# Optimization experiments

Measured on AMD Instinct MI355X. Metric: run time of the kernel, lower is better.

Reference implementation:

```python
import jax, jax.numpy as jnp
import numpy as np

B, S, D = 8, 1024, 1024
H = 2048            # expert hidden dim
E = 8               # num experts
TOP_K = 2
D_NOISE = 256
TEMP = 1.0


def setup_inputs() -> dict:
    key = jax.random.key(0)
    ks = jax.random.split(key, 8)
    return {
        "x": jax.random.normal(ks[0], (B, S, D), dtype=jnp.float32),
        "noise_clock_emb": jax.random.normal(ks[1], (B, D_NOISE), dtype=jnp.float32),
        # router weight [D_noise, E] (xavier-ish scale)
        "route_weight": jax.random.normal(ks[2], (D_NOISE, E), dtype=jnp.float32) * (1.0 / np.sqrt(D_NOISE)),
        # stacked expert params; torch Linear y = x @ W.T + b, stored here pre-transposed
        "fc_in_w": jax.random.normal(ks[3], (E, D, 2 * H), dtype=jnp.float32) * 0.02,
        "fc_in_b": jax.random.normal(ks[4], (E, 2 * H), dtype=jnp.float32) * 0.02,
        "fc_out_w": jax.random.normal(ks[5], (E, H, D), dtype=jnp.float32) * 0.02,
        "fc_out_b": jax.random.normal(ks[6], (E, D), dtype=jnp.float32) * 0.02,
    }


def reference(x, noise_clock_emb, route_weight, fc_in_w, fc_in_b, fc_out_w, fc_out_b):
    # ---- router: P = softmax(phi(sigma) @ W_R / T) ----
    logits = (noise_clock_emb @ route_weight) / TEMP            # [B, E]
    probs = jax.nn.softmax(logits, axis=-1)
    topk_weights, topk_indices = jax.lax.top_k(probs, TOP_K)    # [B, K]
    topk_weights = topk_weights / jnp.clip(
        topk_weights.sum(axis=-1, keepdims=True), 1e-8)
    # dense per-(batch, expert) mixing coefficient, identical to the
    # masked accumulation in the torch loop
    coeff = jnp.einsum("bke,bk->be",
                       jax.nn.one_hot(topk_indices, E, dtype=x.dtype),
                       topk_weights)                             # [B, E]

    # ---- all experts densely over the full batch (matches original math) ----
    h = jnp.einsum("bsd,edh->ebsh", x, fc_in_w) + fc_in_b[:, None, None, :]
    value, gate = jnp.split(h, 2, axis=-1)                       # [E,B,S,H] each
    hidden = value * jax.nn.silu(gate)
    mixed = jnp.einsum("ebsh,ehd,be->bsd", hidden, fc_out_w, coeff)
    mixed = mixed + jnp.einsum("be,ed->bd", coeff, fc_out_b)[:, None, :]
    return mixed, logits, probs, topk_indices, topk_weights
```

## Files before the change

kernel.cpp:

```cpp
#include <hip/hip_runtime.h>
#include <stdint.h>

#define B_ 8
#define S_ 1024
#define D_ 1024
#define H_ 2048
#define E_ 8
#define DN_ 256

typedef unsigned char u8;
typedef unsigned int u32;
typedef float f32x4 __attribute__((ext_vector_type(4)));
typedef long long ll;

__device__ __forceinline__ u8 f2f8(float f) {
  return (u8)(__builtin_amdgcn_cvt_pk_fp8_f32(f, f, 0, false) & 0xff);
}
__device__ __forceinline__ u32 pk4f8(float a, float b, float c, float d) {
  int w = __builtin_amdgcn_cvt_pk_fp8_f32(a, b, 0, false);
  w = __builtin_amdgcn_cvt_pk_fp8_f32(c, d, w, true);
  return (u32)w;
}

__device__ __forceinline__ void gll16(const void* g, void* l) {
  __builtin_amdgcn_global_load_lds(
      (__attribute__((address_space(1))) void*)g,
      (__attribute__((address_space(3))) void*)l, 16, 0, 0);
}

template <int R, int C>
__device__ __forceinline__ void transpose_body(const float* __restrict__ ip,
                                               u8* __restrict__ op,
                                               int bx, int by, int t,
                                               u32 (&tl)[64][65]) {
  const int r0 = by * 256, c0 = bx * 64;
  const int rg16 = t >> 4;
  const int cg = t & 15;
#pragma unroll
  for (int p = 0; p < 4; ++p) {
    const int rq = p * 16 + rg16;
    const float* q = ip + (size_t)(r0 + rq * 4) * C + c0 + cg * 4;
    float4 v0 = *(const float4*)(q);
    float4 v1 = *(const float4*)(q + C);
    float4 v2 = *(const float4*)(q + 2 * C);
    float4 v3 = *(const float4*)(q + 3 * C);
    tl[cg * 4 + 0][rq] = pk4f8(v0.x, v1.x, v2.x, v3.x);
    tl[cg * 4 + 1][rq] = pk4f8(v0.y, v1.y, v2.y, v3.y);
    tl[cg * 4 + 2][rq] = pk4f8(v0.z, v1.z, v2.z, v3.z);
    tl[cg * 4 + 3][rq] = pk4f8(v0.w, v1.w, v2.w, v3.w);
  }
  __syncthreads();
  const int ch = t & 15;
#pragma unroll
  for (int p = 0; p < 4; ++p) {
    const int c = p * 16 + (t >> 4);
    uint4 w;
    w.x = tl[c][ch * 4 + 0];
    w.y = tl[c][ch * 4 + 1];
    w.z = tl[c][ch * 4 + 2];
    w.w = tl[c][ch * 4 + 3];
    *(uint4*)(op + (size_t)(c0 + c) * R + r0 + ch * 16) = w;
  }
}

#define NCAST (B_ * S_ * D_ / 1024)
#define NT1 ((2 * H_ / 64) * (D_ / 256) * E_)
#define NT2 ((D_ / 64) * (H_ / 256) * E_)

__global__ void __launch_bounds__(256) prep_kernel(
    const float* __restrict__ x, const float* __restrict__ noise,
    const float* __restrict__ rw, const float* __restrict__ fiw,
    const float* __restrict__ fow,
    float* __restrict__ out_logits, float* __restrict__ out_probs,
    float* __restrict__ out_idx, float* __restrict__ out_w,
    int* __restrict__ ws_idx, float* __restrict__ ws_w,
    u32* __restrict__ xq, u8* __restrict__ wtin,
    u8* __restrict__ wtout) {
  __shared__ __align__(16) u32 tile[64][65];
  const int t = threadIdx.x;
  int bid = blockIdx.x;

  if (bid == 0) {
    float* sl = (float*)&tile[0][0];
    float* sp = sl + 64;
    {
      const int pair = t >> 2, sub = t & 3;
      const int b = pair >> 3, e = pair & 7;
      float acc = 0.f;
      const int d0 = sub * 64;
      for (int d = d0; d < d0 + 64; ++d)
        acc += noise[b * DN_ + d] * rw[d * E_ + e];
      acc += __shfl_xor(acc, 1);
      acc += __shfl_xor(acc, 2);
      if (sub == 0) sl[pair] = acc;
    }
    __syncthreads();
    if (t < 64) {
      const int b = t >> 3;
      float L = sl[t];
      out_logits[t] = L;
      float m = -1e30f;
      for (int j = 0; j < 8; ++j) m = fmaxf(m, sl[b * 8 + j]);
      float s = 0.f;
      for (int j = 0; j < 8; ++j) s += __expf(sl[b * 8 + j] - m);
      float p = __expf(L - m) / s;
      out_probs[t] = p;
      sp[t] = p;
    }
    __syncthreads();
    if (t < 64 && (t & 7) == 0) {
      const int b = t >> 3;
      int a1 = 0; float v1 = sp[b * 8];
      for (int j = 1; j < 8; ++j) { float v = sp[b * 8 + j]; if (v > v1) { v1 = v; a1 = j; } }
      int a2 = -1; float v2 = -1e30f;
      for (int j = 0; j < 8; ++j) {
        if (j == a1) continue;
        float v = sp[b * 8 + j]; if (v > v2) { v2 = v; a2 = j; }
      }
      float sum = fmaxf(v1 + v2, 1e-8f);
      float w1 = v1 / sum, w2 = v2 / sum;
      out_idx[b * 2] = (float)a1; out_idx[b * 2 + 1] = (float)a2;
      out_w[b * 2] = w1; out_w[b * 2 + 1] = w2;
      ws_idx[b * 2] = a1; ws_idx[b * 2 + 1] = a2;
      ws_w[b * 2] = w1; ws_w[b * 2 + 1] = w2;
    }
    return;
  }
  bid -= 1;
  if (bid < NCAST) {
    const size_t i = (size_t)bid * 256 + t;
    float4 v = *((const float4*)x + i);
    xq[i] = pk4f8(v.x, v.y, v.z, v.w);
    return;
  }
  bid -= NCAST;
  if (bid < NT1) {
    const int bx = bid & 63, by = (bid >> 6) & 3, e = bid >> 8;
    transpose_body<D_, 2 * H_>(fiw + (size_t)e * D_ * 2 * H_,
                               wtin + (size_t)e * D_ * 2 * H_, bx, by, t, tile);
    return;
  }
  bid -= NT1;
  {
    const int bx = bid & 15, by = (bid >> 4) & 7, e = bid >> 7;
    transpose_body<H_, D_>(fow + (size_t)e * H_ * D_,
                           wtout + (size_t)e * H_ * D_, bx, by, t, tile);
  }
}

__global__ void __launch_bounds__(256, 4) gemm1_kernel(
    const u8* __restrict__ xq,
    const u8* __restrict__ wtin,
    const float* __restrict__ bin,
    const int* __restrict__ ws_idx, const float* __restrict__ ws_w,
    u8* __restrict__ hid)
{
  const int nt = blockIdx.x;
  const int mt = blockIdx.y;
  const int z  = blockIdx.z;
  const int b  = z >> 1;
  const int e  = ws_idx[z] & 7;
  const float csc = ws_w[z];

  __shared__ u8 As[128 * 128];
  __shared__ u8 Bs[128 * 128];

  const int t = threadIdx.x;
  const int wave = t >> 6, lane = t & 63;
  const int wm = wave >> 1, wn = wave & 1;
  const int lm = lane & 15, lq = lane >> 4;
  const int lrow8 = lane >> 3;
  const int kq = ((lane & 7) ^ lrow8) * 16;
  const int fsw = lm & 7;
  const int p0 = lq >> 1, fb = (lq & 1) * 8;

  const u8* Ab  = xq + (size_t)b * (S_ * D_) + (size_t)mt * 128 * D_;
  const u8* Bvb = wtin + (size_t)e * (2 * H_ * D_) + (size_t)nt * 64 * D_;
  const u8* Bgb = Bvb + (size_t)H_ * D_;

  const f32x4 vz = {0.f, 0.f, 0.f, 0.f};
  f32x4 accv[4][2], accg[4][2];
#pragma unroll
  for (int i = 0; i < 4; ++i)
#pragma unroll
    for (int j = 0; j < 2; ++j) { accv[i][j] = vz; accg[i][j] = vz; }

  for (int kt = 0; kt < D_ / 128; ++kt) {
    const int k0 = kt * 128 + kq;
    gll16(Ab + (size_t)(wave * 8 + lrow8) * D_ + k0, (char*)As + wave * 1024);
    gll16(Ab + (size_t)((wave + 4) * 8 + lrow8) * D_ + k0, (char*)As + (wave + 4) * 1024);
    gll16(Ab + (size_t)((wave + 8) * 8 + lrow8) * D_ + k0, (char*)As + (wave + 8) * 1024);
    gll16(Ab + (size_t)((wave + 12) * 8 + lrow8) * D_ + k0, (char*)As + (wave + 12) * 1024);
    gll16(Bvb + (size_t)(wave * 8 + lrow8) * D_ + k0, (char*)Bs + wave * 1024);
    gll16(Bvb + (size_t)((wave + 4) * 8 + lrow8) * D_ + k0, (char*)Bs + (wave + 4) * 1024);
    gll16(Bgb + (size_t)(wave * 8 + lrow8) * D_ + k0, (char*)Bs + (8 + wave) * 1024);
    gll16(Bgb + (size_t)((wave + 4) * 8 + lrow8) * D_ + k0, (char*)Bs + (12 + wave) * 1024);
    __syncthreads();
#pragma unroll
    for (int hg = 0; hg < 2; ++hg) {
      ll af[4][2], bvf[2][2], bgf[2][2];
#pragma unroll
      for (int h2 = 0; h2 < 2; ++h2) {
        const int pw = ((((hg * 2 + h2) * 2 + p0) ^ fsw)) * 16 + fb;
#pragma unroll
        for (int i = 0; i < 4; ++i)
          af[i][h2] = *(const ll*)(As + (wm * 64 + i * 16 + lm) * 128 + pw);
#pragma unroll
        for (int j = 0; j < 2; ++j) {
          bvf[j][h2] = *(const ll*)(Bs + (wn * 32 + j * 16 + lm) * 128 + pw);
          bgf[j][h2] = *(const ll*)(Bs + (64 + wn * 32 + j * 16 + lm) * 128 + pw);
        }
      }
#pragma unroll
      for (int h2 = 0; h2 < 2; ++h2)
#pragma unroll
        for (int i = 0; i < 4; ++i)
#pragma unroll
          for (int j = 0; j < 2; ++j) {
            accv[i][j] = __builtin_amdgcn_mfma_f32_16x16x32_fp8_fp8(af[i][h2], bvf[j][h2], accv[i][j], 0, 0, 0);
            accg[i][j] = __builtin_amdgcn_mfma_f32_16x16x32_fp8_fp8(af[i][h2], bgf[j][h2], accg[i][j], 0, 0, 0);
          }
    }
    __syncthreads();
  }

  u8* hb = hid + (size_t)z * (S_ * H_);
  const int row0 = mt * 128 + wm * 64;
  const int col0 = nt * 64 + wn * 32;
#pragma unroll
  for (int j = 0; j < 2; ++j) {
    const int col = col0 + j * 16 + lm;
    const float bvx = bin[e * 2 * H_ + col];
    const float bgx = bin[e * 2 * H_ + H_ + col];
#pragma unroll
    for (int i = 0; i < 4; ++i) {
#pragma unroll
      for (int r = 0; r < 4; ++r) {
        const int srow = row0 + i * 16 + lq * 4 + r;
        float v = accv[i][j][r] + bvx;
        float g = accg[i][j][r] + bgx;
        float hv = v * g / (1.f + __expf(-g)) * csc;
        hb[(size_t)srow * H_ + col] = f2f8(hv);
      }
    }
  }
}

__global__ void __launch_bounds__(256, 4) gemm2_kernel(
    const u8* __restrict__ hid,
    const u8* __restrict__ wtout,
    const float* __restrict__ bout,
    const int* __restrict__ ws_idx, const float* __restrict__ ws_w,
    float* __restrict__ out)
{
  const int nt = blockIdx.x;
  const int mt = blockIdx.y;
  const int b  = blockIdx.z;

  __shared__ u8 As[128 * 128];
  __shared__ u8 Bs[64 * 128];

  const int t = threadIdx.x;
  const int wave = t >> 6, lane = t & 63;
  const int wm = wave >> 1, wn = wave & 1;
  const int lm = lane & 15, lq = lane >> 4;
  const int lrow8 = lane >> 3;
  const int kq = ((lane & 7) ^ lrow8) * 16;
  const int fsw = lm & 7;
  const int p0 = lq >> 1, fb = (lq & 1) * 8;

  const int e0 = ws_idx[b * 2] & 7, e1 = ws_idx[b * 2 + 1] & 7;
  const u8* Ab0 = hid + ((size_t)(b * 2 + 0) * S_ + mt * 128) * H_;
  const u8* Ab1 = hid + ((size_t)(b * 2 + 1) * S_ + mt * 128) * H_;
  const u8* Bb0 = wtout + ((size_t)e0 * D_ + nt * 64) * H_;
  const u8* Bb1 = wtout + ((size_t)e1 * D_ + nt * 64) * H_;

  const f32x4 vz = {0.f, 0.f, 0.f, 0.f};
  f32x4 acc[4][2];
#pragma unroll
  for (int i = 0; i < 4; ++i)
#pragma unroll
    for (int j = 0; j < 2; ++j) acc[i][j] = vz;

  for (int it = 0; it < 32; ++it) {
    const u8* Ab = (it & 16) ? Ab1 : Ab0;
    const u8* Bb = (it & 16) ? Bb1 : Bb0;
    const int k0 = (it & 15) * 128 + kq;
    gll16(Ab + (size_t)(wave * 8 + lrow8) * H_ + k0, (char*)As + wave * 1024);
    gll16(Ab + (size_t)((wave + 4) * 8 + lrow8) * H_ + k0, (char*)As + (wave + 4) * 1024);
    gll16(Ab + (size_t)((wave + 8) * 8 + lrow8) * H_ + k0, (char*)As + (wave + 8) * 1024);
    gll16(Ab + (size_t)((wave + 12) * 8 + lrow8) * H_ + k0, (char*)As + (wave + 12) * 1024);
    gll16(Bb + (size_t)(wave * 8 + lrow8) * H_ + k0, (char*)Bs + wave * 1024);
    gll16(Bb + (size_t)((wave + 4) * 8 + lrow8) * H_ + k0, (char*)Bs + (wave + 4) * 1024);
    __syncthreads();
#pragma unroll
    for (int hg = 0; hg < 2; ++hg) {
      ll af[4][2], bf[2][2];
#pragma unroll
      for (int h2 = 0; h2 < 2; ++h2) {
        const int pw = ((((hg * 2 + h2) * 2 + p0) ^ fsw)) * 16 + fb;
#pragma unroll
        for (int i = 0; i < 4; ++i)
          af[i][h2] = *(const ll*)(As + (wm * 64 + i * 16 + lm) * 128 + pw);
#pragma unroll
        for (int j = 0; j < 2; ++j)
          bf[j][h2] = *(const ll*)(Bs + (wn * 32 + j * 16 + lm) * 128 + pw);
      }
#pragma unroll
      for (int h2 = 0; h2 < 2; ++h2)
#pragma unroll
        for (int i = 0; i < 4; ++i)
#pragma unroll
          for (int j = 0; j < 2; ++j)
            acc[i][j] = __builtin_amdgcn_mfma_f32_16x16x32_fp8_fp8(af[i][h2], bf[j][h2], acc[i][j], 0, 0, 0);
    }
    __syncthreads();
  }

  const float c0 = ws_w[b * 2], c1 = ws_w[b * 2 + 1];
  float* ob = out + (size_t)b * (S_ * D_);
  const int row0 = mt * 128 + wm * 64;
  const int col0 = nt * 64 + wn * 32;
#pragma unroll
  for (int j = 0; j < 2; ++j) {
    const int col = col0 + j * 16 + lm;
    const float bias = c0 * bout[e0 * D_ + col] + c1 * bout[e1 * D_ + col];
#pragma unroll
    for (int i = 0; i < 4; ++i)
#pragma unroll
      for (int r = 0; r < 4; ++r)
        ob[(size_t)(row0 + i * 16 + lq * 4 + r) * D_ + col] = acc[i][j][r] + bias;
  }
}

extern "C" void kernel_launch(void* const* d_in, const int* in_sizes, int n_in,
                              void* d_out, int out_size, void* d_ws, size_t ws_size,
                              hipStream_t stream) {
  const float* x     = (const float*)d_in[0];
  const float* noise = (const float*)d_in[1];
  const float* rw    = (const float*)d_in[2];
  const float* fiw   = (const float*)d_in[3];
  const float* fib   = (const float*)d_in[4];
  const float* fow   = (const float*)d_in[5];
  const float* fob   = (const float*)d_in[6];
  float* out = (float*)d_out;

  char* ws = (char*)d_ws;
  int*   ws_idx = (int*)ws;
  float* ws_w   = (float*)(ws + 64);
  u8* xq    = (u8*)(ws + 256);
  u8* wtin  = xq + (size_t)B_ * S_ * D_;
  u8* wtout = wtin + (size_t)E_ * 2 * H_ * D_;
  u8* hid   = wtout + (size_t)E_ * D_ * H_;

  float* out_mixed  = out;
  float* out_logits = out + (size_t)B_ * S_ * D_;
  float* out_probs  = out_logits + B_ * E_;
  float* out_idx    = out_probs + B_ * E_;
  float* out_w      = out_idx + B_ * 2;

  prep_kernel<<<1 + NCAST + NT1 + NT2, 256, 0, stream>>>(
      x, noise, rw, fiw, fow, out_logits, out_probs, out_idx, out_w,
      ws_idx, ws_w, (u32*)xq, wtin, wtout);
  gemm1_kernel<<<dim3(32, 8, 16), 256, 0, stream>>>(xq, wtin, fib, ws_idx, ws_w, hid);
  gemm2_kernel<<<dim3(16, 8, 8), 256, 0, stream>>>(hid, wtout, fob, ws_idx, ws_w, out_mixed);
}
```

Measured before the change: 425.1 us.

## Share A tile across both selected experts in gemm1 and widen gemm2 N-tile

gemm1 now processes both top-k experts of a batch in one 512-thread block, so the activation tile loaded into shared memory feeds the value and gate projections of both experts. This halves the grid and the activation reloads. gemm2 also moves to 512 threads with a 128-wide output tile, halving its grid and the reloads of the hidden A tile. Each block now uses more LDS (48KB for gemm1) and there are fewer blocks, which could lower occupancy and latency hiding.

```diff
diff --git a/kernel.cpp b/kernel.cpp
--- a/kernel.cpp
+++ b/kernel.cpp
@@ -148,7 +148,7 @@
   }
 }
 
-__global__ void __launch_bounds__(256, 4) gemm1_kernel(
+__global__ void __launch_bounds__(512, 4) gemm1_kernel(
     const u8* __restrict__ xq,
     const u8* __restrict__ wtin,
     const float* __restrict__ bin,
@@ -157,17 +157,16 @@
 {
   const int nt = blockIdx.x;
   const int mt = blockIdx.y;
-  const int z  = blockIdx.z;
-  const int b  = z >> 1;
-  const int e  = ws_idx[z] & 7;
-  const float csc = ws_w[z];
+  const int b  = blockIdx.z;
+  const int e0 = ws_idx[b * 2] & 7, e1 = ws_idx[b * 2 + 1] & 7;
+  const float c0 = ws_w[b * 2], c1 = ws_w[b * 2 + 1];
 
   __shared__ u8 As[128 * 128];
-  __shared__ u8 Bs[128 * 128];
+  __shared__ u8 Bs[256 * 128];
 
   const int t = threadIdx.x;
   const int wave = t >> 6, lane = t & 63;
-  const int wm = wave >> 1, wn = wave & 1;
+  const int wm = wave >> 2, wn = wave & 3;
   const int lm = lane & 15, lq = lane >> 4;
   const int lrow8 = lane >> 3;
   const int kq = ((lane & 7) ^ lrow8) * 16;
@@ -175,78 +174,75 @@
   const int p0 = lq >> 1, fb = (lq & 1) * 8;
 
   const u8* Ab  = xq + (size_t)b * (S_ * D_) + (size_t)mt * 128 * D_;
-  const u8* Bvb = wtin + (size_t)e * (2 * H_ * D_) + (size_t)nt * 64 * D_;
-  const u8* Bgb = Bvb + (size_t)H_ * D_;
+  const u8* Bv0 = wtin + (size_t)e0 * (2 * H_ * D_) + (size_t)nt * 64 * D_;
+  const u8* Bg0 = Bv0 + (size_t)H_ * D_;
+  const u8* Bv1 = wtin + (size_t)e1 * (2 * H_ * D_) + (size_t)nt * 64 * D_;
+  const u8* Bg1 = Bv1 + (size_t)H_ * D_;
 
   const f32x4 vz = {0.f, 0.f, 0.f, 0.f};
-  f32x4 accv[4][2], accg[4][2];
+  f32x4 acc[4][4];
 #pragma unroll
   for (int i = 0; i < 4; ++i)
 #pragma unroll
-    for (int j = 0; j < 2; ++j) { accv[i][j] = vz; accg[i][j] = vz; }
+    for (int j = 0; j < 4; ++j) acc[i][j] = vz;
 
   for (int kt = 0; kt < D_ / 128; ++kt) {
     const int k0 = kt * 128 + kq;
-    gll16(Ab + (size_t)(wave * 8 + lrow8) * D_ + k0, (char*)As + wave * 1024);
-    gll16(Ab + (size_t)((wave + 4) * 8 + lrow8) * D_ + k0, (char*)As + (wave + 4) * 1024);
-    gll16(Ab + (size_t)((wave + 8) * 8 + lrow8) * D_ + k0, (char*)As + (wave + 8) * 1024);
-    gll16(Ab + (size_t)((wave + 12) * 8 + lrow8) * D_ + k0, (char*)As + (wave + 12) * 1024);
-    gll16(Bvb + (size_t)(wave * 8 + lrow8) * D_ + k0, (char*)Bs + wave * 1024);
-    gll16(Bvb + (size_t)((wave + 4) * 8 + lrow8) * D_ + k0, (char*)Bs + (wave + 4) * 1024);
-    gll16(Bgb + (size_t)(wave * 8 + lrow8) * D_ + k0, (char*)Bs + (8 + wave) * 1024);
-    gll16(Bgb + (size_t)((wave + 4) * 8 + lrow8) * D_ + k0, (char*)Bs + (12 + wave) * 1024);
-    __syncthreads();
-#pragma unroll
-    for (int hg = 0; hg < 2; ++hg) {
-      ll af[4][2], bvf[2][2], bgf[2][2];
-#pragma unroll
-      for (int h2 = 0; h2 < 2; ++h2) {
-        const int pw = ((((hg * 2 + h2) * 2 + p0) ^ fsw)) * 16 + fb;
-#pragma unroll
-        for (int i = 0; i < 4; ++i)
-          af[i][h2] = *(const ll*)(As + (wm * 64 + i * 16 + lm) * 128 + pw);
-#pragma unroll
-        for (int j = 0; j < 2; ++j) {
-          bvf[j][h2] = *(const ll*)(Bs + (wn * 32 + j * 16 + lm) * 128 + pw);
-          bgf[j][h2] = *(const ll*)(Bs + (64 + wn * 32 + j * 16 + lm) * 128 + pw);
-        }
+    const size_t rr = (size_t)(wave * 8 + lrow8);
+    gll16(Ab + rr * D_ + k0, (char*)As + wave * 1024);
+    gll16(Ab + (rr + 64) * D_ + k0, (char*)As + (wave + 8) * 1024);
+    gll16(Bv0 + rr * D_ + k0, (char*)Bs + wave * 1024);
+    gll16(Bg0 + rr * D_ + k0, (char*)Bs + (8 + wave) * 1024);
+    gll16(Bv1 + rr * D_ + k0, (char*)Bs + (16 + wave) * 1024);
+    gll16(Bg1 + rr * D_ + k0, (char*)Bs + (24 + wave) * 1024);
+    __syncthreads();
+#pragma unroll
+    for (int ks = 0; ks < 4; ++ks) {
+      const int pw = ((ks * 2 + p0) ^ fsw) * 16 + fb;
+      ll af[4];
+#pragma unroll
+      for (int i = 0; i < 4; ++i)
+        af[i] = *(const ll*)(As + (wm * 64 + i * 16 + lm) * 128 + pw);
+      const int brow = wn * 16 + lm;
+      ll b0v = *(const ll*)(Bs + (brow) * 128 + pw);
+      ll b0g = *(const ll*)(Bs + (64 + brow) * 128 + pw);
+      ll b1v = *(const ll*)(Bs + (128 + brow) * 128 + pw);
+      ll b1g = *(const ll*)(Bs + (192 + brow) * 128 + pw);
+#pragma unroll
+      for (int i = 0; i < 4; ++i) {
+        acc[i][0] = __builtin_amdgcn_mfma_f32_16x16x32_fp8_fp8(af[i], b0v, acc[i][0], 0, 0, 0);
+        acc[i][1] = __builtin_amdgcn_mfma_f32_16x16x32_fp8_fp8(af[i], b0g, acc[i][1], 0, 0, 0);
+        acc[i][2] = __builtin_amdgcn_mfma_f32_16x16x32_fp8_fp8(af[i], b1v, acc[i][2], 0, 0, 0);
+        acc[i][3] = __builtin_amdgcn_mfma_f32_16x16x32_fp8_fp8(af[i], b1g, acc[i][3], 0, 0, 0);
       }
-#pragma unroll
-      for (int h2 = 0; h2 < 2; ++h2)
-#pragma unroll
-        for (int i = 0; i < 4; ++i)
-#pragma unroll
-          for (int j = 0; j < 2; ++j) {
-            accv[i][j] = __builtin_amdgcn_mfma_f32_16x16x32_fp8_fp8(af[i][h2], bvf[j][h2], accv[i][j], 0, 0, 0);
-            accg[i][j] = __builtin_amdgcn_mfma_f32_16x16x32_fp8_fp8(af[i][h2], bgf[j][h2], accg[i][j], 0, 0, 0);
-          }
-    }
-    __syncthreads();
-  }
-
-  u8* hb = hid + (size_t)z * (S_ * H_);
+    }
+    __syncthreads();
+  }
+
+  u8* hb0 = hid + (size_t)(b * 2 + 0) * (S_ * H_);
+  u8* hb1 = hid + (size_t)(b * 2 + 1) * (S_ * H_);
   const int row0 = mt * 128 + wm * 64;
-  const int col0 = nt * 64 + wn * 32;
-#pragma unroll
-  for (int j = 0; j < 2; ++j) {
-    const int col = col0 + j * 16 + lm;
-    const float bvx = bin[e * 2 * H_ + col];
-    const float bgx = bin[e * 2 * H_ + H_ + col];
-#pragma unroll
-    for (int i = 0; i < 4; ++i) {
-#pragma unroll
-      for (int r = 0; r < 4; ++r) {
-        const int srow = row0 + i * 16 + lq * 4 + r;
-        float v = accv[i][j][r] + bvx;
-        float g = accg[i][j][r] + bgx;
-        float hv = v * g / (1.f + __expf(-g)) * csc;
-        hb[(size_t)srow * H_ + col] = f2f8(hv);
-      }
-    }
-  }
-}
-
-__global__ void __launch_bounds__(256, 4) gemm2_kernel(
+  const int col = nt * 64 + wn * 16 + lm;
+  const float bv0 = bin[e0 * 2 * H_ + col];
+  const float bg0 = bin[e0 * 2 * H_ + H_ + col];
+  const float bv1 = bin[e1 * 2 * H_ + col];
+  const float bg1 = bin[e1 * 2 * H_ + H_ + col];
+#pragma unroll
+  for (int i = 0; i < 4; ++i) {
+#pragma unroll
+    for (int r = 0; r < 4; ++r) {
+      const int srow = row0 + i * 16 + lq * 4 + r;
+      float v0 = acc[i][0][r] + bv0;
+      float g0 = acc[i][1][r] + bg0;
+      hb0[(size_t)srow * H_ + col] = f2f8(v0 * g0 / (1.f + __expf(-g0)) * c0);
+      float v1 = acc[i][2][r] + bv1;
+      float g1 = acc[i][3][r] + bg1;
+      hb1[(size_t)srow * H_ + col] = f2f8(v1 * g1 / (1.f + __expf(-g1)) * c1);
+    }
+  }
+}
+
+__global__ void __launch_bounds__(512, 4) gemm2_kernel(
     const u8* __restrict__ hid,
     const u8* __restrict__ wtout,
     const float* __restrict__ bout,
@@ -258,11 +254,11 @@
   const int b  = blockIdx.z;
 
   __shared__ u8 As[128 * 128];
-  __shared__ u8 Bs[64 * 128];
+  __shared__ u8 Bs[128 * 128];
 
   const int t = threadIdx.x;
   const int wave = t >> 6, lane = t & 63;
-  const int wm = wave >> 1, wn = wave & 1;
+  const int wm = wave >> 2, wn = wave & 3;
   const int lm = lane & 15, lq = lane >> 4;
   const int lrow8 = lane >> 3;
   const int kq = ((lane & 7) ^ lrow8) * 16;
@@ -272,8 +268,8 @@
   const int e0 = ws_idx[b * 2] & 7, e1 = ws_idx[b * 2 + 1] & 7;
   const u8* Ab0 = hid + ((size_t)(b * 2 + 0) * S_ + mt * 128) * H_;
   const u8* Ab1 = hid + ((size_t)(b * 2 + 1) * S_ + mt * 128) * H_;
-  const u8* Bb0 = wtout + ((size_t)e0 * D_ + nt * 64) * H_;
-  const u8* Bb1 = wtout + ((size_t)e1 * D_ + nt * 64) * H_;
+  const u8* Bb0 = wtout + ((size_t)e0 * D_ + nt * 128) * H_;
+  const u8* Bb1 = wtout + ((size_t)e1 * D_ + nt * 128) * H_;
 
   const f32x4 vz = {0.f, 0.f, 0.f, 0.f};
   f32x4 acc[4][2];
@@ -286,33 +282,27 @@
     const u8* Ab = (it & 16) ? Ab1 : Ab0;
     const u8* Bb = (it & 16) ? Bb1 : Bb0;
     const int k0 = (it & 15) * 128 + kq;
-    gll16(Ab + (size_t)(wave * 8 + lrow8) * H_ + k0, (char*)As + wave * 1024);
-    gll16(Ab + (size_t)((wave + 4) * 8 + lrow8) * H_ + k0, (char*)As + (wave + 4) * 1024);
-    gll16(Ab + (size_t)((wave + 8) * 8 + lrow8) * H_ + k0, (char*)As + (wave + 8) * 1024);
-    gll16(Ab + (size_t)((wave + 12) * 8 + lrow8) * H_ + k0, (char*)As + (wave + 12) * 1024);
-    gll16(Bb + (size_t)(wave * 8 + lrow8) * H_ + k0, (char*)Bs + wave * 1024);
-    gll16(Bb + (size_t)((wave + 4) * 8 + lrow8) * H_ + k0, (char*)Bs + (wave + 4) * 1024);
-    __syncthreads();
-#pragma unroll
-    for (int hg = 0; hg < 2; ++hg) {
-      ll af[4][2], bf[2][2];
-#pragma unroll
-      for (int h2 = 0; h2 < 2; ++h2) {
-        const int pw = ((((hg * 2 + h2) * 2 + p0) ^ fsw)) * 16 + fb;
-#pragma unroll
-        for (int i = 0; i < 4; ++i)
-          af[i][h2] = *(const ll*)(As + (wm * 64 + i * 16 + lm) * 128 + pw);
+    const size_t rr = (size_t)(wave * 8 + lrow8);
+    gll16(Ab + rr * H_ + k0, (char*)As + wave * 1024);
+    gll16(Ab + (rr + 64) * H_ + k0, (char*)As + (wave + 8) * 1024);
+    gll16(Bb + rr * H_ + k0, (char*)Bs + wave * 1024);
+    gll16(Bb + (rr + 64) * H_ + k0, (char*)Bs + (wave + 8) * 1024);
+    __syncthreads();
+#pragma unroll
+    for (int ks = 0; ks < 4; ++ks) {
+      const int pw = ((ks * 2 + p0) ^ fsw) * 16 + fb;
+      ll af[4], bf[2];
+#pragma unroll
+      for (int i = 0; i < 4; ++i)
+        af[i] = *(const ll*)(As + (wm * 64 + i * 16 + lm) * 128 + pw);
+#pragma unroll
+      for (int j = 0; j < 2; ++j)
+        bf[j] = *(const ll*)(Bs + (wn * 32 + j * 16 + lm) * 128 + pw);
+#pragma unroll
+      for (int i = 0; i < 4; ++i)
 #pragma unroll
         for (int j = 0; j < 2; ++j)
-          bf[j][h2] = *(const ll*)(Bs + (wn * 32 + j * 16 + lm) * 128 + pw);
-      }
-#pragma unroll
-      for (int h2 = 0; h2 < 2; ++h2)
-#pragma unroll
-        for (int i = 0; i < 4; ++i)
-#pragma unroll
-          for (int j = 0; j < 2; ++j)
-            acc[i][j] = __builtin_amdgcn_mfma_f32_16x16x32_fp8_fp8(af[i][h2], bf[j][h2], acc[i][j], 0, 0, 0);
+          acc[i][j] = __builtin_amdgcn_mfma_f32_16x16x32_fp8_fp8(af[i], bf[j], acc[i][j], 0, 0, 0);
     }
     __syncthreads();
   }
@@ -320,7 +310,7 @@
   const float c0 = ws_w[b * 2], c1 = ws_w[b * 2 + 1];
   float* ob = out + (size_t)b * (S_ * D_);
   const int row0 = mt * 128 + wm * 64;
-  const int col0 = nt * 64 + wn * 32;
+  const int col0 = nt * 128 + wn * 32;
 #pragma unroll
   for (int j = 0; j < 2; ++j) {
     const int col = col0 + j * 16 + lm;
@@ -362,6 +352,6 @@
   prep_kernel<<<1 + NCAST + NT1 + NT2, 256, 0, stream>>>(
       x, noise, rw, fiw, fow, out_logits, out_probs, out_idx, out_w,
       ws_idx, ws_w, (u32*)xq, wtin, wtout);
-  gemm1_kernel<<<dim3(32, 8, 16), 256, 0, stream>>>(xq, wtin, fib, ws_idx, ws_w, hid);
-  gemm2_kernel<<<dim3(16, 8, 8), 256, 0, stream>>>(hid, wtout, fob, ws_idx, ws_w, out_mixed);
-}
+  gemm1_kernel<<<dim3(32, 8, 8), 512, 0, stream>>>(xq, wtin, fib, ws_idx, ws_w, hid);
+  gemm2_kernel<<<dim3(8, 8, 8), 512, 0, stream>>>(hid, wtout, fob, ws_idx, ws_w, out_mixed);
+}
```

After: 446.4 us. 5.0% more time.
